# Performance work log

Hardware: AMD Instinct MI355X
Metric: run time of the kernel (lower is better)

## Reference

```python
import jax, jax.numpy as jnp
import numpy as np

N_NODES = 50000
N_EDGES = 640000
IN_CH = 128
OUT_CH = 128
HID = 2 * OUT_CH  # 256


def _glorot(key, shape):
    fan_in, fan_out = shape
    lim = np.sqrt(6.0 / (fan_in + fan_out)).astype(np.float32)
    return jax.random.uniform(key, shape, jnp.float32, -lim, lim)


def setup_inputs() -> dict:
    key = jax.random.key(0)
    ks = jax.random.split(key, 8)
    x = jax.random.normal(ks[0], (N_NODES, IN_CH), jnp.float32)
    edge_index = jax.random.randint(ks[1], (2, N_EDGES), 0, N_NODES, jnp.int64)
    # SAGEConv layer 1: lin_l (neighbor branch, with bias), lin_r (root branch, no bias)
    w1_l = _glorot(ks[2], (IN_CH, HID))
    b1_l = jnp.zeros((HID,), jnp.float32)
    w1_r = _glorot(ks[3], (IN_CH, HID))
    # SAGEConv layer 2
    w2_l = _glorot(ks[4], (HID, OUT_CH))
    b2_l = jnp.zeros((OUT_CH,), jnp.float32)
    w2_r = _glorot(ks[5], (HID, OUT_CH))
    return {"x": x, "edge_index": edge_index,
            "w1_l": w1_l, "b1_l": b1_l, "w1_r": w1_r,
            "w2_l": w2_l, "b2_l": b2_l, "w2_r": w2_r}


def _sage_conv(x, src, dst, w_l, b_l, w_r):
    # mean aggregation of source-node features onto destination nodes
    msgs = x[src]                                       # [E, C] gather
    agg = jax.ops.segment_sum(msgs, dst, num_segments=N_NODES)  # [N, C]
    cnt = jax.ops.segment_sum(jnp.ones((src.shape[0],), x.dtype), dst,
                              num_segments=N_NODES)     # [N]
    mean = agg / jnp.maximum(cnt, 1.0)[:, None]
    # out = lin_l(mean_neighbors) + lin_r(x_root)
    return mean @ w_l + b_l + x @ w_r


def reference(x, edge_index, w1_l, b1_l, w1_r, w2_l, b2_l, w2_r):
    src, dst = edge_index[0], edge_index[1]
    h = _sage_conv(x, src, dst, w1_l, b1_l, w1_r)
    h = jax.nn.relu(h)
    return _sage_conv(h, src, dst, w2_l, b2_l, w2_r)
```

## Files before the change

### kernel.cpp

```cpp
#include <hip/hip_runtime.h>

#define N_NODES 50000
#define N_EDGES 640000
#define IN_CH 128
#define OUT_CH 128
#define HID 256
#define M_PAD 50048
#define CAP 64

typedef unsigned int uint;
typedef unsigned short ushort;

__device__ __forceinline__ ushort f2b(float f) {
    uint u = __float_as_uint(f);
    u += 0x7FFFu + ((u >> 16) & 1u);
    return (ushort)(u >> 16);
}
__device__ __forceinline__ float b2f_lo(uint u) { return __uint_as_float(u << 16); }
__device__ __forceinline__ float b2f_hi(uint u) { return __uint_as_float(u & 0xFFFF0000u); }
__device__ __forceinline__ uint packb(float lo, float hi) {
    return (uint)f2b(lo) | ((uint)f2b(hi) << 16);
}

__device__ __forceinline__ void gload_lds16(const ushort* g, ushort* l) {
    __builtin_amdgcn_global_load_lds(
        (const __attribute__((address_space(1))) void*)g,
        (__attribute__((address_space(3))) void*)l, 16, 0, 0);
}

__global__ __launch_bounds__(256) void prep(
    const int* __restrict__ src, const int* __restrict__ dst,
    const float* __restrict__ x, const float* __restrict__ w1l,
    const float* __restrict__ w1r, const float* __restrict__ w2l,
    const float* __restrict__ w2r, int* __restrict__ cnt,
    int* __restrict__ col, ushort* __restrict__ xcat,
    ushort* __restrict__ w1f, ushort* __restrict__ w2f) {
    int b = blockIdx.x;
    if (b < 2500) {
        int e = b * 256 + threadIdx.x;
        int d = dst[e];
        int p = atomicAdd(&cnt[d], 1);
        if (p < CAP) col[d * CAP + p] = src[e];
    } else {
        int id = (b - 2500) * 256 + threadIdx.x;
        if (id < 800000) {
            long long base = (long long)id * 8;
            float4 a = *(const float4*)(x + base);
            float4 c = *(const float4*)(x + base + 4);
            uint4 o;
            o.x = packb(a.x, a.y);
            o.y = packb(a.z, a.w);
            o.z = packb(c.x, c.y);
            o.w = packb(c.z, c.w);
            int row = id >> 4;
            int cc = id & 15;
            ((uint4*)xcat)[(size_t)row * 32 + 16 + cc] = o;
        } else if (id < 865536) {
            int i = id - 800000;
            int n0 = i >> 12, kk = (i >> 9) & 7, lane = (i >> 3) & 63, j = i & 7;
            int n = n0 * 16 + (lane & 15);
            int k = kk * 32 + (lane >> 4) * 8 + j;
            float v = (k < 128) ? w1l[k * 256 + n] : w1r[(k - 128) * 256 + n];
            w1f[i] = f2b(v);
        } else {
            int i = id - 865536;
            int n0 = i >> 12, kk = (i >> 9) & 7, lane = (i >> 3) & 63, j = i & 7;
            int n = n0 * 16 + (lane & 15);
            int k = kk * 32 + (lane >> 4) * 8 + j;
            float v = (n < 128) ? w2l[k * 128 + n] : w2r[k * 128 + (n - 128)];
            w2f[i] = f2b(v);
        }
    }
}

__global__ __launch_bounds__(256) void aggregate_mean1(
    const int* __restrict__ cnt, const int* __restrict__ col,
    ushort* __restrict__ xcat) {
    int t = blockIdx.x * 256 + threadIdx.x;
    int node = t >> 4;
    int q = t & 15;
    if (node >= N_NODES) return;
    int degf = cnt[node];
    int deg = min(degf, CAP);
    const int* cb = col + node * CAP;
    float acc[8] = {0.f, 0.f, 0.f, 0.f, 0.f, 0.f, 0.f, 0.f};
    const uint4* f4 = (const uint4*)xcat;
    int j = 0;
    for (; j + 4 <= deg; j += 4) {
        int4 s4 = *(const int4*)(cb + j);
        uint4 v0 = f4[(size_t)s4.x * 32 + 16 + q];
        uint4 v1 = f4[(size_t)s4.y * 32 + 16 + q];
        uint4 v2 = f4[(size_t)s4.z * 32 + 16 + q];
        uint4 v3 = f4[(size_t)s4.w * 32 + 16 + q];
        acc[0] += b2f_lo(v0.x) + b2f_lo(v1.x) + b2f_lo(v2.x) + b2f_lo(v3.x);
        acc[1] += b2f_hi(v0.x) + b2f_hi(v1.x) + b2f_hi(v2.x) + b2f_hi(v3.x);
        acc[2] += b2f_lo(v0.y) + b2f_lo(v1.y) + b2f_lo(v2.y) + b2f_lo(v3.y);
        acc[3] += b2f_hi(v0.y) + b2f_hi(v1.y) + b2f_hi(v2.y) + b2f_hi(v3.y);
        acc[4] += b2f_lo(v0.z) + b2f_lo(v1.z) + b2f_lo(v2.z) + b2f_lo(v3.z);
        acc[5] += b2f_hi(v0.z) + b2f_hi(v1.z) + b2f_hi(v2.z) + b2f_hi(v3.z);
        acc[6] += b2f_lo(v0.w) + b2f_lo(v1.w) + b2f_lo(v2.w) + b2f_lo(v3.w);
        acc[7] += b2f_hi(v0.w) + b2f_hi(v1.w) + b2f_hi(v2.w) + b2f_hi(v3.w);
    }
    for (; j < deg; ++j) {
        uint4 v = f4[(size_t)cb[j] * 32 + 16 + q];
        acc[0] += b2f_lo(v.x); acc[1] += b2f_hi(v.x);
        acc[2] += b2f_lo(v.y); acc[3] += b2f_hi(v.y);
        acc[4] += b2f_lo(v.z); acc[5] += b2f_hi(v.z);
        acc[6] += b2f_lo(v.w); acc[7] += b2f_hi(v.w);
    }
    float inv = 1.0f / fmaxf((float)degf, 1.0f);
    uint4 o;
    o.x = packb(acc[0] * inv, acc[1] * inv);
    o.y = packb(acc[2] * inv, acc[3] * inv);
    o.z = packb(acc[4] * inv, acc[5] * inv);
    o.w = packb(acc[6] * inv, acc[7] * inv);
    ((uint4*)xcat)[(size_t)node * 32 + q] = o;
}

__global__ __launch_bounds__(256) void combine2(
    const ushort* __restrict__ hw, const int* __restrict__ cnt,
    const int* __restrict__ col, const float* __restrict__ bias,
    float* __restrict__ out) {
    int t = blockIdx.x * 256 + threadIdx.x;
    int node = t >> 4;
    int q = t & 15;
    if (node >= N_NODES) return;
    int degf = cnt[node];
    int deg = min(degf, CAP);
    const int* cb = col + node * CAP;
    float acc[8] = {0.f, 0.f, 0.f, 0.f, 0.f, 0.f, 0.f, 0.f};
    const uint4* f4 = (const uint4*)hw;
    int j = 0;
    for (; j + 4 <= deg; j += 4) {
        int4 s4 = *(const int4*)(cb + j);
        uint4 v0 = f4[(size_t)s4.x * 32 + q];
        uint4 v1 = f4[(size_t)s4.y * 32 + q];
        uint4 v2 = f4[(size_t)s4.z * 32 + q];
        uint4 v3 = f4[(size_t)s4.w * 32 + q];
        acc[0] += b2f_lo(v0.x) + b2f_lo(v1.x) + b2f_lo(v2.x) + b2f_lo(v3.x);
        acc[1] += b2f_hi(v0.x) + b2f_hi(v1.x) + b2f_hi(v2.x) + b2f_hi(v3.x);
        acc[2] += b2f_lo(v0.y) + b2f_lo(v1.y) + b2f_lo(v2.y) + b2f_lo(v3.y);
        acc[3] += b2f_hi(v0.y) + b2f_hi(v1.y) + b2f_hi(v2.y) + b2f_hi(v3.y);
        acc[4] += b2f_lo(v0.z) + b2f_lo(v1.z) + b2f_lo(v2.z) + b2f_lo(v3.z);
        acc[5] += b2f_hi(v0.z) + b2f_hi(v1.z) + b2f_hi(v2.z) + b2f_hi(v3.z);
        acc[6] += b2f_lo(v0.w) + b2f_lo(v1.w) + b2f_lo(v2.w) + b2f_lo(v3.w);
        acc[7] += b2f_hi(v0.w) + b2f_hi(v1.w) + b2f_hi(v2.w) + b2f_hi(v3.w);
    }
    for (; j < deg; ++j) {
        uint4 v = f4[(size_t)cb[j] * 32 + q];
        acc[0] += b2f_lo(v.x); acc[1] += b2f_hi(v.x);
        acc[2] += b2f_lo(v.y); acc[3] += b2f_hi(v.y);
        acc[4] += b2f_lo(v.z); acc[5] += b2f_hi(v.z);
        acc[6] += b2f_lo(v.w); acc[7] += b2f_hi(v.w);
    }
    float inv = 1.0f / fmaxf((float)degf, 1.0f);
    uint4 r = f4[(size_t)node * 32 + 16 + q];
    float4 b0 = *(const float4*)(bias + q * 8);
    float4 b1 = *(const float4*)(bias + q * 8 + 4);
    float4 o0, o1;
    o0.x = acc[0] * inv + b2f_lo(r.x) + b0.x;
    o0.y = acc[1] * inv + b2f_hi(r.x) + b0.y;
    o0.z = acc[2] * inv + b2f_lo(r.y) + b0.z;
    o0.w = acc[3] * inv + b2f_hi(r.y) + b0.w;
    o1.x = acc[4] * inv + b2f_lo(r.z) + b1.x;
    o1.y = acc[5] * inv + b2f_hi(r.z) + b1.y;
    o1.z = acc[6] * inv + b2f_lo(r.w) + b1.z;
    o1.w = acc[7] * inv + b2f_hi(r.w) + b1.w;
    *(float4*)(out + (size_t)node * 128 + q * 8) = o0;
    *(float4*)(out + (size_t)node * 128 + q * 8 + 4) = o1;
}

using bf16x8 = __attribute__((ext_vector_type(8))) short;
using f32x4  = __attribute__((ext_vector_type(4))) float;

__global__ __launch_bounds__(256) void fused_gemm(
    const ushort* __restrict__ A, const ushort* __restrict__ w1f,
    const ushort* __restrict__ w2f, const float* __restrict__ b1,
    ushort* __restrict__ hw) {
    __shared__ alignas(16) ushort tile[32 * 256];

    const int tid = threadIdx.x;
    const int lane = tid & 63;
    const int wave = tid >> 6;
    const int quad = lane >> 4;
    const int l16 = lane & 15;
    const int bm = blockIdx.x * 32;

#pragma unroll
    for (int r = 0; r < 4; ++r) {
        int row = r * 8 + (tid >> 5);
        int c = tid & 31;
        int src = (c & 24) | ((c & 7) ^ (row & 7));
        gload_lds16(A + (size_t)(bm + row) * 256 + src * 8, &tile[row * 256 + c * 8]);
    }

    f32x4 acc[2][4];
#pragma unroll
    for (int rt = 0; rt < 2; ++rt)
#pragma unroll
        for (int ct = 0; ct < 4; ++ct) acc[rt][ct] = (f32x4){0.f, 0.f, 0.f, 0.f};

    const size_t bstep = 64 * 8;
    const ushort* w1b = w1f + (((size_t)(wave * 4) * 8) * 64 + lane) * 8;
    const ushort* w2b = w2f + (((size_t)(wave * 4) * 8) * 64 + lane) * 8;

    bf16x8 bc[4], bn[4];
#pragma unroll
    for (int ct = 0; ct < 4; ++ct)
        bc[ct] = *(const bf16x8*)(w1b + (size_t)ct * 8 * bstep);

    __syncthreads();

#pragma unroll
    for (int kk = 0; kk < 8; ++kk) {
        if (kk < 7) {
#pragma unroll
            for (int ct = 0; ct < 4; ++ct)
                bn[ct] = *(const bf16x8*)(w1b + ((size_t)ct * 8 + kk + 1) * bstep);
        }
        bf16x8 af[2];
#pragma unroll
        for (int rt = 0; rt < 2; ++rt) {
            int row = rt * 16 + l16;
            int c = kk * 4 + quad;
            int slot = (c & 24) | ((c & 7) ^ (row & 7));
            af[rt] = *(const bf16x8*)&tile[row * 256 + slot * 8];
        }
#pragma unroll
        for (int ct = 0; ct < 4; ++ct) {
#pragma unroll
            for (int rt = 0; rt < 2; ++rt)
                acc[rt][ct] = __builtin_amdgcn_mfma_f32_16x16x32_bf16(
                    af[rt], bc[ct], acc[rt][ct], 0, 0, 0);
        }
#pragma unroll
        for (int ct = 0; ct < 4; ++ct) bc[ct] = bn[ct];
    }
    __syncthreads();

#pragma unroll
    for (int ct = 0; ct < 4; ++ct) {
        int colg = wave * 64 + ct * 16 + l16;
        float bv = b1[colg];
        int cc = colg >> 3;
        int off = colg & 7;
#pragma unroll
        for (int rt = 0; rt < 2; ++rt) {
#pragma unroll
            for (int reg = 0; reg < 4; ++reg) {
                int row = rt * 16 + quad * 4 + reg;
                int slot = (cc & 24) | ((cc & 7) ^ (row & 7));
                tile[row * 256 + slot * 8 + off] = f2b(fmaxf(acc[rt][ct][reg] + bv, 0.0f));
            }
        }
    }

#pragma unroll
    for (int rt = 0; rt < 2; ++rt)
#pragma unroll
        for (int ct = 0; ct < 4; ++ct) acc[rt][ct] = (f32x4){0.f, 0.f, 0.f, 0.f};

#pragma unroll
    for (int ct = 0; ct < 4; ++ct)
        bc[ct] = *(const bf16x8*)(w2b + (size_t)ct * 8 * bstep);

    __syncthreads();

#pragma unroll
    for (int kk = 0; kk < 8; ++kk) {
        if (kk < 7) {
#pragma unroll
            for (int ct = 0; ct < 4; ++ct)
                bn[ct] = *(const bf16x8*)(w2b + ((size_t)ct * 8 + kk + 1) * bstep);
        }
        bf16x8 af[2];
#pragma unroll
        for (int rt = 0; rt < 2; ++rt) {
            int row = rt * 16 + l16;
            int c = kk * 4 + quad;
            int slot = (c & 24) | ((c & 7) ^ (row & 7));
            af[rt] = *(const bf16x8*)&tile[row * 256 + slot * 8];
        }
#pragma unroll
        for (int ct = 0; ct < 4; ++ct) {
#pragma unroll
            for (int rt = 0; rt < 2; ++rt)
                acc[rt][ct] = __builtin_amdgcn_mfma_f32_16x16x32_bf16(
                    af[rt], bc[ct], acc[rt][ct], 0, 0, 0);
        }
#pragma unroll
        for (int ct = 0; ct < 4; ++ct) bc[ct] = bn[ct];
    }
    __syncthreads();

#pragma unroll
    for (int ct = 0; ct < 4; ++ct) {
        int colg = wave * 64 + ct * 16 + l16;
        int cc = colg >> 3;
        int off = colg & 7;
#pragma unroll
        for (int rt = 0; rt < 2; ++rt) {
#pragma unroll
            for (int reg = 0; reg < 4; ++reg) {
                int row = rt * 16 + quad * 4 + reg;
                int slot = (cc & 24) | ((cc & 7) ^ (row & 7));
                tile[row * 256 + slot * 8 + off] = f2b(acc[rt][ct][reg]);
            }
        }
    }
    __syncthreads();
#pragma unroll
    for (int r = 0; r < 4; ++r) {
        int row = r * 8 + (tid >> 5);
        int c = tid & 31;
        int slot = (c & 24) | ((c & 7) ^ (row & 7));
        uint4 v = *(const uint4*)&tile[row * 256 + slot * 8];
        *(uint4*)(hw + (size_t)(bm + row) * 256 + c * 8) = v;
    }
}

extern "C" void kernel_launch(void* const* d_in, const int* in_sizes, int n_in,
                              void* d_out, int out_size, void* d_ws, size_t ws_size,
                              hipStream_t stream) {
    const float* x    = (const float*)d_in[0];
    const int*   ei   = (const int*)d_in[1];
    const float* w1_l = (const float*)d_in[2];
    const float* b1_l = (const float*)d_in[3];
    const float* w1_r = (const float*)d_in[4];
    const float* w2_l = (const float*)d_in[5];
    const float* b2_l = (const float*)d_in[6];
    const float* w2_r = (const float*)d_in[7];
    float* out = (float*)d_out;

    const int* src = ei;
    const int* dst = ei + N_EDGES;

    int* cnt = (int*)d_ws;
    int* col = cnt + N_NODES;
    size_t int_bytes = (size_t)(N_NODES + N_NODES * CAP) * 4;
    size_t ofs = (int_bytes + 15) & ~(size_t)15;
    ushort* xcat = (ushort*)((char*)d_ws + ofs);
    ushort* hw   = xcat + (size_t)M_PAD * HID;
    ushort* w1f  = hw + (size_t)M_PAD * HID;
    ushort* w2f  = w1f + HID * HID;

    hipMemsetAsync(cnt, 0, (size_t)N_NODES * sizeof(int), stream);

    prep<<<6137, 256, 0, stream>>>(src, dst, x, w1_l, w1_r, w2_l, w2_r,
                                   cnt, col, xcat, w1f, w2f);

    aggregate_mean1<<<N_NODES * 16 / 256, 256, 0, stream>>>(cnt, col, xcat);
    fused_gemm<<<M_PAD / 32, 256, 0, stream>>>(xcat, w1f, w2f, b1_l, hw);
    combine2<<<N_NODES * 16 / 256, 256, 0, stream>>>(hw, cnt, col, b2_l, out);
}
```

Measured before the change: 230.2 us.

## Partition neighbor gathers by source-node range and widen per-thread feature slices

```diff
diff --git a/kernel.cpp b/kernel.cpp
--- a/kernel.cpp
+++ b/kernel.cpp
@@ -77,44 +77,45 @@
     const int* __restrict__ cnt, const int* __restrict__ col,
     ushort* __restrict__ xcat) {
     int t = blockIdx.x * 256 + threadIdx.x;
-    int node = t >> 4;
-    int q = t & 15;
+    int node = t >> 3;
+    int q8 = t & 7;
     if (node >= N_NODES) return;
     int degf = cnt[node];
     int deg = min(degf, CAP);
     const int* cb = col + node * CAP;
-    float acc[8] = {0.f, 0.f, 0.f, 0.f, 0.f, 0.f, 0.f, 0.f};
     const uint4* f4 = (const uint4*)xcat;
-    int j = 0;
-    for (; j + 4 <= deg; j += 4) {
-        int4 s4 = *(const int4*)(cb + j);
-        uint4 v0 = f4[(size_t)s4.x * 32 + 16 + q];
-        uint4 v1 = f4[(size_t)s4.y * 32 + 16 + q];
-        uint4 v2 = f4[(size_t)s4.z * 32 + 16 + q];
-        uint4 v3 = f4[(size_t)s4.w * 32 + 16 + q];
-        acc[0] += b2f_lo(v0.x) + b2f_lo(v1.x) + b2f_lo(v2.x) + b2f_lo(v3.x);
-        acc[1] += b2f_hi(v0.x) + b2f_hi(v1.x) + b2f_hi(v2.x) + b2f_hi(v3.x);
-        acc[2] += b2f_lo(v0.y) + b2f_lo(v1.y) + b2f_lo(v2.y) + b2f_lo(v3.y);
-        acc[3] += b2f_hi(v0.y) + b2f_hi(v1.y) + b2f_hi(v2.y) + b2f_hi(v3.y);
-        acc[4] += b2f_lo(v0.z) + b2f_lo(v1.z) + b2f_lo(v2.z) + b2f_lo(v3.z);
-        acc[5] += b2f_hi(v0.z) + b2f_hi(v1.z) + b2f_hi(v2.z) + b2f_hi(v3.z);
-        acc[6] += b2f_lo(v0.w) + b2f_lo(v1.w) + b2f_lo(v2.w) + b2f_lo(v3.w);
-        acc[7] += b2f_hi(v0.w) + b2f_hi(v1.w) + b2f_hi(v2.w) + b2f_hi(v3.w);
-    }
-    for (; j < deg; ++j) {
-        uint4 v = f4[(size_t)cb[j] * 32 + 16 + q];
-        acc[0] += b2f_lo(v.x); acc[1] += b2f_hi(v.x);
-        acc[2] += b2f_lo(v.y); acc[3] += b2f_hi(v.y);
-        acc[4] += b2f_lo(v.z); acc[5] += b2f_hi(v.z);
-        acc[6] += b2f_lo(v.w); acc[7] += b2f_hi(v.w);
+    float acc[16];
+#pragma unroll
+    for (int i = 0; i < 16; ++i) acc[i] = 0.f;
+    for (int p = 0; p < 7; ++p) {
+        for (int j = 0; j < deg; ++j) {
+            int s = cb[j];
+            if ((s >> 13) == p) {
+                uint4 a0 = f4[(size_t)s * 32 + 16 + q8 * 2];
+                uint4 a1 = f4[(size_t)s * 32 + 17 + q8 * 2];
+                acc[0] += b2f_lo(a0.x);  acc[1] += b2f_hi(a0.x);
+                acc[2] += b2f_lo(a0.y);  acc[3] += b2f_hi(a0.y);
+                acc[4] += b2f_lo(a0.z);  acc[5] += b2f_hi(a0.z);
+                acc[6] += b2f_lo(a0.w);  acc[7] += b2f_hi(a0.w);
+                acc[8]  += b2f_lo(a1.x); acc[9]  += b2f_hi(a1.x);
+                acc[10] += b2f_lo(a1.y); acc[11] += b2f_hi(a1.y);
+                acc[12] += b2f_lo(a1.z); acc[13] += b2f_hi(a1.z);
+                acc[14] += b2f_lo(a1.w); acc[15] += b2f_hi(a1.w);
+            }
+        }
     }
     float inv = 1.0f / fmaxf((float)degf, 1.0f);
-    uint4 o;
-    o.x = packb(acc[0] * inv, acc[1] * inv);
-    o.y = packb(acc[2] * inv, acc[3] * inv);
-    o.z = packb(acc[4] * inv, acc[5] * inv);
-    o.w = packb(acc[6] * inv, acc[7] * inv);
-    ((uint4*)xcat)[(size_t)node * 32 + q] = o;
+    uint4 o0, o1;
+    o0.x = packb(acc[0] * inv, acc[1] * inv);
+    o0.y = packb(acc[2] * inv, acc[3] * inv);
+    o0.z = packb(acc[4] * inv, acc[5] * inv);
+    o0.w = packb(acc[6] * inv, acc[7] * inv);
+    o1.x = packb(acc[8] * inv, acc[9] * inv);
+    o1.y = packb(acc[10] * inv, acc[11] * inv);
+    o1.z = packb(acc[12] * inv, acc[13] * inv);
+    o1.w = packb(acc[14] * inv, acc[15] * inv);
+    ((uint4*)xcat)[(size_t)node * 32 + q8 * 2] = o0;
+    ((uint4*)xcat)[(size_t)node * 32 + q8 * 2 + 1] = o1;
 }
 
 __global__ __launch_bounds__(256) void combine2(
@@ -122,52 +123,62 @@
     const int* __restrict__ col, const float* __restrict__ bias,
     float* __restrict__ out) {
     int t = blockIdx.x * 256 + threadIdx.x;
-    int node = t >> 4;
-    int q = t & 15;
+    int node = t >> 3;
+    int q8 = t & 7;
     if (node >= N_NODES) return;
     int degf = cnt[node];
     int deg = min(degf, CAP);
     const int* cb = col + node * CAP;
-    float acc[8] = {0.f, 0.f, 0.f, 0.f, 0.f, 0.f, 0.f, 0.f};
     const uint4* f4 = (const uint4*)hw;
-    int j = 0;
-    for (; j + 4 <= deg; j += 4) {
-        int4 s4 = *(const int4*)(cb + j);
-        uint4 v0 = f4[(size_t)s4.x * 32 + q];
-        uint4 v1 = f4[(size_t)s4.y * 32 + q];
-        uint4 v2 = f4[(size_t)s4.z * 32 + q];
-        uint4 v3 = f4[(size_t)s4.w * 32 + q];
-        acc[0] += b2f_lo(v0.x) + b2f_lo(v1.x) + b2f_lo(v2.x) + b2f_lo(v3.x);
-        acc[1] += b2f_hi(v0.x) + b2f_hi(v1.x) + b2f_hi(v2.x) + b2f_hi(v3.x);
-        acc[2] += b2f_lo(v0.y) + b2f_lo(v1.y) + b2f_lo(v2.y) + b2f_lo(v3.y);
-        acc[3] += b2f_hi(v0.y) + b2f_hi(v1.y) + b2f_hi(v2.y) + b2f_hi(v3.y);
-        acc[4] += b2f_lo(v0.z) + b2f_lo(v1.z) + b2f_lo(v2.z) + b2f_lo(v3.z);
-        acc[5] += b2f_hi(v0.z) + b2f_hi(v1.z) + b2f_hi(v2.z) + b2f_hi(v3.z);
-        acc[6] += b2f_lo(v0.w) + b2f_lo(v1.w) + b2f_lo(v2.w) + b2f_lo(v3.w);
-        acc[7] += b2f_hi(v0.w) + b2f_hi(v1.w) + b2f_hi(v2.w) + b2f_hi(v3.w);
-    }
-    for (; j < deg; ++j) {
-        uint4 v = f4[(size_t)cb[j] * 32 + q];
-        acc[0] += b2f_lo(v.x); acc[1] += b2f_hi(v.x);
-        acc[2] += b2f_lo(v.y); acc[3] += b2f_hi(v.y);
-        acc[4] += b2f_lo(v.z); acc[5] += b2f_hi(v.z);
-        acc[6] += b2f_lo(v.w); acc[7] += b2f_hi(v.w);
+    float acc[16];
+#pragma unroll
+    for (int i = 0; i < 16; ++i) acc[i] = 0.f;
+    for (int p = 0; p < 7; ++p) {
+        for (int j = 0; j < deg; ++j) {
+            int s = cb[j];
+            if ((s >> 13) == p) {
+                uint4 a0 = f4[(size_t)s * 32 + q8 * 2];
+                uint4 a1 = f4[(size_t)s * 32 + q8 * 2 + 1];
+                acc[0] += b2f_lo(a0.x);  acc[1] += b2f_hi(a0.x);
+                acc[2] += b2f_lo(a0.y);  acc[3] += b2f_hi(a0.y);
+                acc[4] += b2f_lo(a0.z);  acc[5] += b2f_hi(a0.z);
+                acc[6] += b2f_lo(a0.w);  acc[7] += b2f_hi(a0.w);
+                acc[8]  += b2f_lo(a1.x); acc[9]  += b2f_hi(a1.x);
+                acc[10] += b2f_lo(a1.y); acc[11] += b2f_hi(a1.y);
+                acc[12] += b2f_lo(a1.z); acc[13] += b2f_hi(a1.z);
+                acc[14] += b2f_lo(a1.w); acc[15] += b2f_hi(a1.w);
+            }
+        }
     }
     float inv = 1.0f / fmaxf((float)degf, 1.0f);
-    uint4 r = f4[(size_t)node * 32 + 16 + q];
-    float4 b0 = *(const float4*)(bias + q * 8);
-    float4 b1 = *(const float4*)(bias + q * 8 + 4);
-    float4 o0, o1;
-    o0.x = acc[0] * inv + b2f_lo(r.x) + b0.x;
-    o0.y = acc[1] * inv + b2f_hi(r.x) + b0.y;
-    o0.z = acc[2] * inv + b2f_lo(r.y) + b0.z;
-    o0.w = acc[3] * inv + b2f_hi(r.y) + b0.w;
-    o1.x = acc[4] * inv + b2f_lo(r.z) + b1.x;
-    o1.y = acc[5] * inv + b2f_hi(r.z) + b1.y;
-    o1.z = acc[6] * inv + b2f_lo(r.w) + b1.z;
-    o1.w = acc[7] * inv + b2f_hi(r.w) + b1.w;
-    *(float4*)(out + (size_t)node * 128 + q * 8) = o0;
-    *(float4*)(out + (size_t)node * 128 + q * 8 + 4) = o1;
+    uint4 r0 = f4[(size_t)node * 32 + 16 + q8 * 2];
+    uint4 r1 = f4[(size_t)node * 32 + 17 + q8 * 2];
+    int c0 = q8 * 16;
+    float4 b0 = *(const float4*)(bias + c0);
+    float4 b1 = *(const float4*)(bias + c0 + 4);
+    float4 b2 = *(const float4*)(bias + c0 + 8);
+    float4 b3 = *(const float4*)(bias + c0 + 12);
+    float4 o0, o1, o2, o3;
+    o0.x = acc[0] * inv + b2f_lo(r0.x) + b0.x;
+    o0.y = acc[1] * inv + b2f_hi(r0.x) + b0.y;
+    o0.z = acc[2] * inv + b2f_lo(r0.y) + b0.z;
+    o0.w = acc[3] * inv + b2f_hi(r0.y) + b0.w;
+    o1.x = acc[4] * inv + b2f_lo(r0.z) + b1.x;
+    o1.y = acc[5] * inv + b2f_hi(r0.z) + b1.y;
+    o1.z = acc[6] * inv + b2f_lo(r0.w) + b1.z;
+    o1.w = acc[7] * inv + b2f_hi(r0.w) + b1.w;
+    o2.x = acc[8] * inv + b2f_lo(r1.x) + b2.x;
+    o2.y = acc[9] * inv + b2f_hi(r1.x) + b2.y;
+    o2.z = acc[10] * inv + b2f_lo(r1.y) + b2.z;
+    o2.w = acc[11] * inv + b2f_hi(r1.y) + b2.w;
+    o3.x = acc[12] * inv + b2f_lo(r1.z) + b3.x;
+    o3.y = acc[13] * inv + b2f_hi(r1.z) + b3.y;
+    o3.z = acc[14] * inv + b2f_lo(r1.w) + b3.z;
+    o3.w = acc[15] * inv + b2f_hi(r1.w) + b3.w;
+    *(float4*)(out + (size_t)node * 128 + c0) = o0;
+    *(float4*)(out + (size_t)node * 128 + c0 + 4) = o1;
+    *(float4*)(out + (size_t)node * 128 + c0 + 8) = o2;
+    *(float4*)(out + (size_t)node * 128 + c0 + 12) = o3;
 }
 
 using bf16x8 = __attribute__((ext_vector_type(8))) short;
@@ -346,10 +357,10 @@
 
     hipMemsetAsync(cnt, 0, (size_t)N_NODES * sizeof(int), stream);
 
-    prep<<<6137, 256, 0, stream>>>(src, dst, x, w1_l, w1_r, w2_l, w2_r,
-                                   cnt, col, xcat, w1f, w2f);
-
-    aggregate_mean1<<<N_NODES * 16 / 256, 256, 0, stream>>>(cnt, col, xcat);
+    prep<<<2500 + 3637, 256, 0, stream>>>(src, dst, x, w1_l, w1_r, w2_l, w2_r,
+                                          cnt, col, xcat, w1f, w2f);
+
+    aggregate_mean1<<<(N_NODES * 8 + 255) / 256, 256, 0, stream>>>(cnt, col, xcat);
     fused_gemm<<<M_PAD / 32, 256, 0, stream>>>(xcat, w1f, w2f, b1_l, hw);
-    combine2<<<N_NODES * 16 / 256, 256, 0, stream>>>(hw, cnt, col, b2_l, out);
-}
+    combine2<<<(N_NODES * 8 + 255) / 256, 256, 0, stream>>>(hw, cnt, col, b2_l, out);
+}
```

Measured after the change: 329.6 us. +43.2%, slower.

## Build neighbor lists with sliced counts, prefix bases, and a second fill pass

Applied to the files above, without the earlier changes.

```diff
diff --git a/kernel.cpp b/kernel.cpp
--- a/kernel.cpp
+++ b/kernel.cpp
@@ -29,18 +29,17 @@
 }
 
 __global__ __launch_bounds__(256) void prep(
-    const int* __restrict__ src, const int* __restrict__ dst,
-    const float* __restrict__ x, const float* __restrict__ w1l,
-    const float* __restrict__ w1r, const float* __restrict__ w2l,
-    const float* __restrict__ w2r, int* __restrict__ cnt,
-    int* __restrict__ col, ushort* __restrict__ xcat,
+    const int* __restrict__ dst, const float* __restrict__ x,
+    const float* __restrict__ w1l, const float* __restrict__ w1r,
+    const float* __restrict__ w2l, const float* __restrict__ w2r,
+    int* __restrict__ cnt8, ushort* __restrict__ xcat,
     ushort* __restrict__ w1f, ushort* __restrict__ w2f) {
     int b = blockIdx.x;
     if (b < 2500) {
         int e = b * 256 + threadIdx.x;
         int d = dst[e];
-        int p = atomicAdd(&cnt[d], 1);
-        if (p < CAP) col[d * CAP + p] = src[e];
+        int s = b & 7;
+        atomicAdd(&cnt8[s * N_NODES + d], 1);
     } else {
         int id = (b - 2500) * 256 + threadIdx.x;
         if (id < 800000) {
@@ -73,6 +72,32 @@
     }
 }
 
+__global__ __launch_bounds__(256) void bases(
+    const int* __restrict__ cnt8, int* __restrict__ pos8,
+    int* __restrict__ cnt) {
+    int node = blockIdx.x * 256 + threadIdx.x;
+    if (node >= N_NODES) return;
+    int run = 0;
+#pragma unroll
+    for (int s = 0; s < 8; ++s) {
+        int c = cnt8[s * N_NODES + node];
+        pos8[s * N_NODES + node] = run;
+        run += c;
+    }
+    cnt[node] = run;
+}
+
+__global__ __launch_bounds__(256) void prep2(
+    const int* __restrict__ src, const int* __restrict__ dst,
+    int* __restrict__ pos8, int* __restrict__ col) {
+    int b = blockIdx.x;
+    int e = b * 256 + threadIdx.x;
+    int d = dst[e];
+    int s = b & 7;
+    int p = atomicAdd(&pos8[s * N_NODES + d], 1);
+    if (p < CAP) col[d * CAP + p] = src[e];
+}
+
 __global__ __launch_bounds__(256) void aggregate_mean1(
     const int* __restrict__ cnt, const int* __restrict__ col,
     ushort* __restrict__ xcat) {
@@ -335,19 +360,23 @@
     const int* src = ei;
     const int* dst = ei + N_EDGES;
 
-    int* cnt = (int*)d_ws;
-    int* col = cnt + N_NODES;
-    size_t int_bytes = (size_t)(N_NODES + N_NODES * CAP) * 4;
+    int* cnt  = (int*)d_ws;
+    int* cnt8 = cnt + N_NODES;
+    int* pos8 = cnt8 + 8 * N_NODES;
+    int* col  = pos8 + 8 * N_NODES;
+    size_t int_bytes = (size_t)(N_NODES * 17 + N_NODES * CAP) * 4;
     size_t ofs = (int_bytes + 15) & ~(size_t)15;
     ushort* xcat = (ushort*)((char*)d_ws + ofs);
     ushort* hw   = xcat + (size_t)M_PAD * HID;
     ushort* w1f  = hw + (size_t)M_PAD * HID;
     ushort* w2f  = w1f + HID * HID;
 
-    hipMemsetAsync(cnt, 0, (size_t)N_NODES * sizeof(int), stream);
-
-    prep<<<6137, 256, 0, stream>>>(src, dst, x, w1_l, w1_r, w2_l, w2_r,
-                                   cnt, col, xcat, w1f, w2f);
+    hipMemsetAsync(cnt8, 0, (size_t)8 * N_NODES * sizeof(int), stream);
+
+    prep<<<2500 + 3637, 256, 0, stream>>>(dst, x, w1_l, w1_r, w2_l, w2_r,
+                                          cnt8, xcat, w1f, w2f);
+    bases<<<196, 256, 0, stream>>>(cnt8, pos8, cnt);
+    prep2<<<2500, 256, 0, stream>>>(src, dst, pos8, col);
 
     aggregate_mean1<<<N_NODES * 16 / 256, 256, 0, stream>>>(cnt, col, xcat);
     fused_gemm<<<M_PAD / 32, 256, 0, stream>>>(xcat, w1f, w2f, b1_l, hw);
```

Result: slower. 250.0 us (+8.6%).
